# Optimization experiments

Measured on AMD Instinct MI355X. Metric: run time of the kernel, lower is better.

The kernel has to match this reference:

```python
import jax, jax.numpy as jnp
import numpy as np

B, C, H, W = 4, 256, 64, 64
C8 = C // 8


def _xavier(key, shape):
    fan_in, fan_out = shape[1], shape[0]
    limit = float(np.sqrt(6.0 / (fan_in + fan_out)))
    return jax.random.uniform(key, shape, jnp.float32, -limit, limit)


def setup_inputs() -> dict:
    key = jax.random.key(0)
    ks = jax.random.split(key, 10)
    inp = {
        "x": jax.random.normal(ks[0], (B, C, H, W), jnp.float32),
        "y": jax.random.normal(ks[1], (B, C, H, W), jnp.float32),
        "Wfx": _xavier(ks[2], (C8, C)), "bfx": jnp.zeros((C8,), jnp.float32),
        "Wgx": _xavier(ks[3], (C8, C)), "bgx": jnp.zeros((C8,), jnp.float32),
        "Whx": _xavier(ks[4], (C, C)),  "bhx": jnp.zeros((C,), jnp.float32),
        "Wfy": _xavier(ks[5], (C8, C)), "bfy": jnp.zeros((C8,), jnp.float32),
        "Wgy": _xavier(ks[6], (C8, C)), "bgy": jnp.zeros((C8,), jnp.float32),
        "Why": _xavier(ks[7], (C, C)),  "bhy": jnp.zeros((C,), jnp.float32),
        # torch init is gamma=0 which zeroes the attention branch; use a random
        # scalar so the reference exercises the full computation.
        "gamma": jax.random.normal(ks[8], (1,), jnp.float32),
    }
    return inp


def _conv1x1(x, Wt, b):
    # 1x1 conv == per-pixel linear over channels; output flattened to [B, O, N]
    b_, c, h, w = x.shape
    out = jnp.einsum('oc,bchw->bohw', Wt, x) + b[None, :, None, None]
    return out.reshape(b_, -1, h * w)


def reference(x, y, Wfx, bfx, Wgx, bgx, Whx, bhx, Wfy, bfy, Wgy, bgy, Why, bhy, gamma):
    b, c, h, w = x.shape
    fx = _conv1x1(x, Wfx, bfx)  # [B, C8, N]
    gx = _conv1x1(x, Wgx, bgx)
    hx = _conv1x1(x, Whx, bhx)  # [B, C, N]
    fy = _conv1x1(y, Wfy, bfy)
    gy = _conv1x1(y, Wgy, bgy)
    hy = _conv1x1(y, Why, bhy)

    # attention_x = softmax(f_y^T @ g_x) over last dim; [B, N, N]
    att_x = jax.nn.softmax(jnp.einsum('bcn,bcm->bnm', fy, gx), axis=-1)
    att_y = jax.nn.softmax(jnp.einsum('bcn,bcm->bnm', fx, gy), axis=-1)

    sa_x = jnp.einsum('bcn,bnm->bcm', hx, att_x).reshape(b, c, h, w)
    sa_y = jnp.einsum('bcn,bnm->bcm', hy, att_y).reshape(b, c, h, w)

    out_x = gamma[0] * sa_x + x
    out_y = gamma[0] * sa_y + y
    return (out_x, out_y)
```

## Files before the change

kernel.cpp:

```cpp
#include <hip/hip_runtime.h>

#define BB 4
#define CC 256
#define NN 4096

typedef _Float16 half_t;
typedef __attribute__((ext_vector_type(8))) _Float16 half8;
typedef __attribute__((ext_vector_type(4))) _Float16 half4;
typedef __attribute__((ext_vector_type(4))) float floatx4;
typedef __attribute__((ext_vector_type(16))) float floatx16;

__global__ __launch_bounds__(256)
void cvt_w_kernel(const float* __restrict__ Wfx, const float* __restrict__ Wgx,
                  const float* __restrict__ Whx, const float* __restrict__ Wfy,
                  const float* __restrict__ Wgy, const float* __restrict__ Why,
                  half_t* __restrict__ oWfx, half_t* __restrict__ oWgx,
                  half_t* __restrict__ oWhx, half_t* __restrict__ oWfy,
                  half_t* __restrict__ oWgy, half_t* __restrict__ oWhy)
{
    const float* src; half_t* dst; int n;
    switch (blockIdx.y) {
        case 0: src = Wfx; dst = oWfx; n = 32 * CC; break;
        case 1: src = Wgx; dst = oWgx; n = 32 * CC; break;
        case 2: src = Whx; dst = oWhx; n = CC * CC; break;
        case 3: src = Wfy; dst = oWfy; n = 32 * CC; break;
        case 4: src = Wgy; dst = oWgy; n = 32 * CC; break;
        default: src = Why; dst = oWhy; n = CC * CC; break;
    }
    int idx = (blockIdx.x * 256 + threadIdx.x) * 4;
    if (idx >= n) return;
    float4 v = *(const float4*)&src[idx];
    half4 h; h[0] = (half_t)v.x; h[1] = (half_t)v.y; h[2] = (half_t)v.z; h[3] = (half_t)v.w;
    *(half4*)&dst[idx] = h;
}

__global__ __launch_bounds__(256)
void transpose_cvt_kernel(const float* __restrict__ x, const float* __restrict__ y,
                          half_t* __restrict__ xTx, half_t* __restrict__ xTy)
{
    const int n0 = blockIdx.x * 64;
    const int c0 = blockIdx.y * 64;
    const int b  = blockIdx.z & 3;
    const int sel = blockIdx.z >> 2;
    const float* in = sel ? y : x;
    half_t* outT = sel ? xTy : xTx;
    const int t  = threadIdx.x;
    const int ch = t & 7, nl = t >> 3;
    const float* inb = in + (size_t)b * CC * NN;
    half_t* outb = outT + (size_t)b * NN * CC;

    #pragma unroll
    for (int p = 0; p < 2; ++p) {
        int n = n0 + nl + 32 * p;
        half8 hv;
        #pragma unroll
        for (int j = 0; j < 8; ++j)
            hv[j] = (half_t)inb[(size_t)(c0 + 8 * ch + j) * NN + n];
        *(half8*)&outb[(size_t)n * CC + c0 + 8 * ch] = hv;
    }
}

__global__ __launch_bounds__(256)
void proj_fg_kernel(const half_t* __restrict__ xTx, const half_t* __restrict__ xTy,
                    const half_t* __restrict__ Wfx, const half_t* __restrict__ Wgx,
                    const half_t* __restrict__ Wfy, const half_t* __restrict__ Wgy,
                    const float* __restrict__ bfx, const float* __restrict__ bgx,
                    const float* __restrict__ bfy, const float* __restrict__ bgy,
                    half_t* __restrict__ fxT, half_t* __restrict__ gxT,
                    half_t* __restrict__ fyT, half_t* __restrict__ gyT)
{
    const int n0 = blockIdx.x * 64;
    const int b  = blockIdx.y;
    const int sel = blockIdx.z;
    const half_t* xT = sel ? xTy : xTx;
    const half_t* Wf = sel ? Wfy : Wfx;
    const half_t* Wg = sel ? Wgy : Wgx;
    const float*  bf = sel ? bfy : bfx;
    const float*  bg = sel ? bgy : bgx;
    half_t* fT = sel ? fyT : fxT;
    half_t* gT = sel ? gyT : gxT;

    const int t  = threadIdx.x;
    const int w = t >> 6, lane = t & 63, q = lane >> 4, mc = lane & 15;
    const half_t* xTb = xT + (size_t)b * NN * CC;

    floatx4 acc[4];
    #pragma unroll
    for (int i = 0; i < 4; ++i) {
        float bv = (i < 2 ? bf : bg)[(i & 1) * 16 + mc];
        acc[i] = (floatx4){bv, bv, bv, bv};
    }

    #pragma unroll
    for (int ks = 0; ks < 8; ++ks) {
        int k0 = ks * 32 + q * 8;
        half8 af = *(const half8*)&xTb[(size_t)(n0 + w * 16 + mc) * CC + k0];
        #pragma unroll
        for (int i = 0; i < 4; ++i) {
            const half_t* Ws = (i < 2) ? Wf : Wg;
            half8 bfr = *(const half8*)&Ws[(size_t)((i & 1) * 16 + mc) * CC + k0];
            acc[i] = __builtin_amdgcn_mfma_f32_16x16x32_f16(af, bfr, acc[i], 0, 0, 0);
        }
    }

    #pragma unroll
    for (int i = 0; i < 4; ++i) {
        half_t* dst = (i < 2) ? fT : gT;
        #pragma unroll
        for (int r = 0; r < 4; ++r) {
            int n = n0 + w * 16 + q * 4 + r;
            dst[((size_t)b * NN + n) * 32 + (i & 1) * 16 + mc] = (half_t)acc[i][r];
        }
    }
}

__global__ __launch_bounds__(256)
void proj_h_kernel(const half_t* __restrict__ xTx, const half_t* __restrict__ xTy,
                   const half_t* __restrict__ Whx, const half_t* __restrict__ Why,
                   const float* __restrict__ bhx, const float* __restrict__ bhy,
                   half_t* __restrict__ hx, half_t* __restrict__ hy)
{
    const int n0 = blockIdx.x * 64;
    const int o0 = blockIdx.y * 128;
    const int b  = blockIdx.z & 3;
    const int sel = blockIdx.z >> 2;
    const half_t* xT = sel ? xTy : xTx;
    const half_t* Wh = sel ? Why : Whx;
    const float*  bh = sel ? bhy : bhx;
    half_t* h = sel ? hy : hx;

    const int t  = threadIdx.x;
    const int w = t >> 6, lane = t & 63, q = lane >> 4, mc = lane & 15;
    const half_t* xTb = xT + (size_t)b * NN * CC;
    half_t* hb = h + (size_t)b * CC * NN;

    floatx4 acc[2][4];
    #pragma unroll
    for (int j = 0; j < 2; ++j) {
        floatx4 bv;
        #pragma unroll
        for (int r = 0; r < 4; ++r) bv[r] = bh[o0 + w * 32 + j * 16 + q * 4 + r];
        #pragma unroll
        for (int i = 0; i < 4; ++i) acc[j][i] = bv;
    }

    #pragma unroll
    for (int ks = 0; ks < 8; ++ks) {
        int k0 = ks * 32 + q * 8;
        half8 a0 = *(const half8*)&Wh[(size_t)(o0 + w * 32 + mc) * CC + k0];
        half8 a1 = *(const half8*)&Wh[(size_t)(o0 + w * 32 + 16 + mc) * CC + k0];
        #pragma unroll
        for (int i = 0; i < 4; ++i) {
            half8 bfr = *(const half8*)&xTb[(size_t)(n0 + i * 16 + mc) * CC + k0];
            acc[0][i] = __builtin_amdgcn_mfma_f32_16x16x32_f16(a0, bfr, acc[0][i], 0, 0, 0);
            acc[1][i] = __builtin_amdgcn_mfma_f32_16x16x32_f16(a1, bfr, acc[1][i], 0, 0, 0);
        }
    }

    #pragma unroll
    for (int j = 0; j < 2; ++j)
        #pragma unroll
        for (int i = 0; i < 4; ++i)
            #pragma unroll
            for (int r = 0; r < 4; ++r) {
                int o = o0 + w * 32 + j * 16 + q * 4 + r;
                hb[(size_t)o * NN + n0 + i * 16 + mc] = (half_t)acc[j][i][r];
            }
}

__global__ __launch_bounds__(256)
void stats_kernel(const half_t* __restrict__ fT0, const half_t* __restrict__ gT0,
                  const half_t* __restrict__ fT1, const half_t* __restrict__ gT1,
                  float* __restrict__ L0, float* __restrict__ L1)
{
    __shared__ float red_l[4][32];
    const int b  = blockIdx.y;
    const int sel = blockIdx.z;
    const half_t* fT = sel ? fT1 : fT0;
    const half_t* gT = sel ? gT1 : gT0;
    float* Lout = sel ? L1 : L0;

    const int n0 = blockIdx.x * 32;
    const int t  = threadIdx.x;
    const int w = t >> 6, lane = t & 63, q = lane >> 4, mc = lane & 15;
    const half_t* fTb = fT + (size_t)b * NN * 32;
    const half_t* gTb = gT + (size_t)b * NN * 32;

    half8 a0 = *(const half8*)&fTb[(size_t)(n0 + mc) * 32 + q * 8];
    half8 a1 = *(const half8*)&fTb[(size_t)(n0 + 16 + mc) * 32 + q * 8];

    float l0[4] = {0.f, 0.f, 0.f, 0.f}, l1[4] = {0.f, 0.f, 0.f, 0.f};
    for (int it = 0; it < NN / 64; ++it) {
        int m = (it * 4 + w) * 16 + mc;
        half8 bfr = *(const half8*)&gTb[(size_t)m * 32 + q * 8];
        floatx4 S0 = __builtin_amdgcn_mfma_f32_16x16x32_f16(a0, bfr, (floatx4){0.f,0.f,0.f,0.f}, 0, 0, 0);
        floatx4 S1 = __builtin_amdgcn_mfma_f32_16x16x32_f16(a1, bfr, (floatx4){0.f,0.f,0.f,0.f}, 0, 0, 0);
        #pragma unroll
        for (int r = 0; r < 4; ++r) { l0[r] += __expf(S0[r]); l1[r] += __expf(S1[r]); }
    }
    #pragma unroll
    for (int r = 0; r < 4; ++r) {
        #pragma unroll
        for (int off = 1; off < 16; off <<= 1) {
            l0[r] += __shfl_xor(l0[r], off);
            l1[r] += __shfl_xor(l1[r], off);
        }
    }
    if (mc == 0)
        #pragma unroll
        for (int r = 0; r < 4; ++r) {
            red_l[w][q * 4 + r]      = l0[r];
            red_l[w][16 + q * 4 + r] = l1[r];
        }
    __syncthreads();
    if (t < 32) {
        float L = red_l[0][t] + red_l[1][t] + red_l[2][t] + red_l[3][t];
        Lout[(size_t)b * NN + n0 + t] = -log2f(L);
    }
}

__global__ __launch_bounds__(512, 4)
void pv_kernel(const half_t* __restrict__ fT0, const half_t* __restrict__ gT0,
               const half_t* __restrict__ h0, const float* __restrict__ L0,
               const float* __restrict__ src0, float* __restrict__ out0,
               const half_t* __restrict__ fT1, const half_t* __restrict__ gT1,
               const half_t* __restrict__ h1, const float* __restrict__ L1,
               const float* __restrict__ src1, float* __restrict__ out1,
               const float* __restrict__ gamma)
{
    __shared__ half_t h_lds[256][72];
    __shared__ half_t PT[2][64][72];

    const int m0 = blockIdx.x * 64;
    const int b  = blockIdx.y & 3;
    const int sel = blockIdx.y >> 2;
    const half_t* fT = sel ? fT1 : fT0;
    const half_t* gT = sel ? gT1 : gT0;
    const half_t* h  = sel ? h1 : h0;
    const float*  Lg = sel ? L1 : L0;
    const float*  src = sel ? src1 : src0;
    float* out = sel ? out1 : out0;

    const int t = threadIdx.x;
    const int w = t >> 6, lane = t & 63;
    const int q = lane >> 4, mc = lane & 15;
    const int l5 = lane >> 5, l31 = lane & 31;

    const int mg  = (w >> 1) * 16;
    const int nhf = (w & 1) * 32;

    const half_t* fTb = fT + (size_t)b * NN * 32;
    const half_t* gTb = gT + (size_t)b * NN * 32;
    const half_t* hb  = h + (size_t)b * CC * NN;
    const float*  Lb  = Lg + (size_t)b * NN;

    const half8 gS = *(const half8*)&gTb[(size_t)(m0 + mg + mc) * 32 + q * 8];

    const int srow = t >> 3;
    const int sch  = t & 7;

    const half_t* hP = hb + (size_t)srow * NN + sch * 8;
    const half_t* fP = fTb + (size_t)(nhf + mc) * 32 + q * 8;
    const float*  lP = Lb + nhf + q * 4;

    floatx16 acc[2];
    #pragma unroll
    for (int bm = 0; bm < 2; ++bm)
        #pragma unroll
        for (int r = 0; r < 16; ++r) acc[bm][r] = 0.f;

    half8 hpre[4];
    half8 fu[2], ff[2];
    floatx4 lvu[2], lvf[2];

    {
        half8 f0[2]; floatx4 l0[2];
        #pragma unroll
        for (int s = 0; s < 2; ++s) {
            f0[s] = *(const half8*)&fP[(size_t)(s * 16) * 32];
            l0[s] = *(const floatx4*)&lP[s * 16];
        }
        #pragma unroll
        for (int s = 0; s < 2; ++s) {
            floatx4 S = __builtin_amdgcn_mfma_f32_16x16x32_f16(
                f0[s], gS, (floatx4){0.f, 0.f, 0.f, 0.f}, 0, 0, 0);
            half4 p;
            p[0] = (half_t)exp2f(fmaf(S[0], 1.44269504f, l0[s][0]));
            p[1] = (half_t)exp2f(fmaf(S[1], 1.44269504f, l0[s][1]));
            p[2] = (half_t)exp2f(fmaf(S[2], 1.44269504f, l0[s][2]));
            p[3] = (half_t)exp2f(fmaf(S[3], 1.44269504f, l0[s][3]));
            *(half4*)&PT[0][mg + mc][nhf + s * 16 + q * 4] = p;
        }
    }
    #pragma unroll
    for (int i = 0; i < 4; ++i)
        hpre[i] = *(const half8*)&hP[(size_t)(64 * i) * NN];
    #pragma unroll
    for (int s = 0; s < 2; ++s) {
        fu[s]  = *(const half8*)&fP[(size_t)(64 + s * 16) * 32];
        lvu[s] = *(const floatx4*)&lP[64 + s * 16];
    }

    #pragma unroll 2
    for (int T = 0; T < NN / 64; ++T) {
        const int cur = T & 1, nxt = cur ^ 1;

        __syncthreads();
        #pragma unroll
        for (int i = 0; i < 4; ++i)
            *(half8*)&h_lds[srow + 64 * i][sch * 8] = hpre[i];
        __syncthreads();

        int ntn  = (T + 1) * 64; if (ntn  >= NN) ntn  = 0;
        int ntn2 = (T + 2) * 64; if (ntn2 >= NN) ntn2 -= NN;
        #pragma unroll
        for (int i = 0; i < 4; ++i)
            hpre[i] = *(const half8*)&hP[(size_t)(64 * i) * NN + ntn];
        #pragma unroll
        for (int s = 0; s < 2; ++s) {
            ff[s]  = *(const half8*)&fP[(size_t)(ntn2 + s * 16) * 32];
            lvf[s] = *(const floatx4*)&lP[ntn2 + s * 16];
        }

        #pragma unroll
        for (int s = 0; s < 2; ++s) {
            floatx4 S = __builtin_amdgcn_mfma_f32_16x16x32_f16(
                fu[s], gS, (floatx4){0.f, 0.f, 0.f, 0.f}, 0, 0, 0);
            half4 p;
            p[0] = (half_t)exp2f(fmaf(S[0], 1.44269504f, lvu[s][0]));
            p[1] = (half_t)exp2f(fmaf(S[1], 1.44269504f, lvu[s][1]));
            p[2] = (half_t)exp2f(fmaf(S[2], 1.44269504f, lvu[s][2]));
            p[3] = (half_t)exp2f(fmaf(S[3], 1.44269504f, lvu[s][3]));
            *(half4*)&PT[nxt][mg + mc][nhf + s * 16 + q * 4] = p;
        }

        __builtin_amdgcn_s_setprio(1);
        #pragma unroll
        for (int ch = 0; ch < 4; ++ch) {
            half8 Ah = *(const half8*)&h_lds[w * 32 + l31][ch * 16 + l5 * 8];
            half8 B0 = *(const half8*)&PT[cur][l31][ch * 16 + l5 * 8];
            half8 B1 = *(const half8*)&PT[cur][32 + l31][ch * 16 + l5 * 8];
            acc[0] = __builtin_amdgcn_mfma_f32_32x32x16_f16(Ah, B0, acc[0], 0, 0, 0);
            acc[1] = __builtin_amdgcn_mfma_f32_32x32x16_f16(Ah, B1, acc[1], 0, 0, 0);
        }
        __builtin_amdgcn_s_setprio(0);

        #pragma unroll
        for (int s = 0; s < 2; ++s) { fu[s] = ff[s]; lvu[s] = lvf[s]; }
    }

    const float gm = gamma[0];
    const float* srcb = src + (size_t)b * CC * NN;
    float* outb = out + (size_t)b * CC * NN;
    #pragma unroll
    for (int bm = 0; bm < 2; ++bm) {
        const int m = m0 + bm * 32 + l31;
        #pragma unroll
        for (int r = 0; r < 16; ++r) {
            int c = w * 32 + (r & 3) + 8 * (r >> 2) + 4 * l5;
            size_t idx = (size_t)c * NN + m;
            outb[idx] = fmaf(gm, acc[bm][r], srcb[idx]);
        }
    }
}

extern "C" void kernel_launch(void* const* d_in, const int* in_sizes, int n_in,
                              void* d_out, int out_size, void* d_ws, size_t ws_size,
                              hipStream_t stream)
{
    const float* x   = (const float*)d_in[0];
    const float* y   = (const float*)d_in[1];
    const float* Wfx = (const float*)d_in[2];
    const float* bfx = (const float*)d_in[3];
    const float* Wgx = (const float*)d_in[4];
    const float* bgx = (const float*)d_in[5];
    const float* Whx = (const float*)d_in[6];
    const float* bhx = (const float*)d_in[7];
    const float* Wfy = (const float*)d_in[8];
    const float* bfy = (const float*)d_in[9];
    const float* Wgy = (const float*)d_in[10];
    const float* bgy = (const float*)d_in[11];
    const float* Why = (const float*)d_in[12];
    const float* bhy = (const float*)d_in[13];
    const float* gam = (const float*)d_in[14];

    const size_t SZ_XT = (size_t)BB * NN * CC;
    const size_t SZ_FG = (size_t)BB * NN * 32;
    half_t* xTx   = (half_t*)d_ws;
    half_t* xTy   = xTx + SZ_XT;
    half_t* hx    = xTy + SZ_XT;
    half_t* hy    = hx + SZ_XT;
    half_t* fxT   = hy + SZ_XT;
    half_t* gxT   = fxT + SZ_FG;
    half_t* fyT   = gxT + SZ_FG;
    half_t* gyT   = fyT + SZ_FG;
    half_t* Wfx_h = gyT + SZ_FG;
    half_t* Wgx_h = Wfx_h + 32 * CC;
    half_t* Wfy_h = Wgx_h + 32 * CC;
    half_t* Wgy_h = Wfy_h + 32 * CC;
    half_t* Whx_h = Wgy_h + 32 * CC;
    half_t* Why_h = Whx_h + CC * CC;
    float*  Lx    = (float*)(Why_h + CC * CC);
    float*  Ly    = Lx + (size_t)BB * NN;

    float* outx = (float*)d_out;
    float* outy = outx + (size_t)BB * CC * NN;

    cvt_w_kernel<<<dim3(64, 6), 256, 0, stream>>>(Wfx, Wgx, Whx, Wfy, Wgy, Why,
                                                  Wfx_h, Wgx_h, Whx_h, Wfy_h, Wgy_h, Why_h);

    transpose_cvt_kernel<<<dim3(64, 4, 8), 256, 0, stream>>>(x, y, xTx, xTy);

    proj_fg_kernel<<<dim3(64, 4, 2), 256, 0, stream>>>(
        xTx, xTy, Wfx_h, Wgx_h, Wfy_h, Wgy_h, bfx, bgx, bfy, bgy, fxT, gxT, fyT, gyT);

    proj_h_kernel<<<dim3(64, 2, 8), 256, 0, stream>>>(
        xTx, xTy, Whx_h, Why_h, bhx, bhy, hx, hy);

    stats_kernel<<<dim3(128, 4, 2), 256, 0, stream>>>(fyT, gxT, fxT, gyT, Lx, Ly);

    pv_kernel<<<dim3(64, 8), 512, 0, stream>>>(
        fyT, gxT, hx, Lx, x, outx,
        fxT, gyT, hy, Ly, y, outy, gam);
}
```

Baseline: 282.9 us.

## Fuse transpose-convert and f/g/h projections into one LDS-staged prep kernel

Result: faster. 253.4 us (-10.4%).

```diff
diff --git a/kernel.cpp b/kernel.cpp
--- a/kernel.cpp
+++ b/kernel.cpp
@@ -34,138 +34,119 @@
     *(half4*)&dst[idx] = h;
 }
 
-__global__ __launch_bounds__(256)
-void transpose_cvt_kernel(const float* __restrict__ x, const float* __restrict__ y,
-                          half_t* __restrict__ xTx, half_t* __restrict__ xTy)
+__global__ __launch_bounds__(512, 4)
+void prep_kernel(const float* __restrict__ x, const float* __restrict__ y,
+                 const half_t* __restrict__ Wfx, const half_t* __restrict__ Wgx,
+                 const half_t* __restrict__ Whx, const half_t* __restrict__ Wfy,
+                 const half_t* __restrict__ Wgy, const half_t* __restrict__ Why,
+                 const float* __restrict__ bfx, const float* __restrict__ bgx,
+                 const float* __restrict__ bhx, const float* __restrict__ bfy,
+                 const float* __restrict__ bgy, const float* __restrict__ bhy,
+                 half_t* __restrict__ fxT, half_t* __restrict__ gxT,
+                 half_t* __restrict__ hx,
+                 half_t* __restrict__ fyT, half_t* __restrict__ gyT,
+                 half_t* __restrict__ hy)
 {
-    const int n0 = blockIdx.x * 64;
-    const int c0 = blockIdx.y * 64;
-    const int b  = blockIdx.z & 3;
-    const int sel = blockIdx.z >> 2;
-    const float* in = sel ? y : x;
-    half_t* outT = sel ? xTy : xTx;
-    const int t  = threadIdx.x;
-    const int ch = t & 7, nl = t >> 3;
-    const float* inb = in + (size_t)b * CC * NN;
-    half_t* outb = outT + (size_t)b * NN * CC;
-
-    #pragma unroll
-    for (int p = 0; p < 2; ++p) {
-        int n = n0 + nl + 32 * p;
-        half8 hv;
-        #pragma unroll
-        for (int j = 0; j < 8; ++j)
-            hv[j] = (half_t)inb[(size_t)(c0 + 8 * ch + j) * NN + n];
-        *(half8*)&outb[(size_t)n * CC + c0 + 8 * ch] = hv;
-    }
-}
-
-__global__ __launch_bounds__(256)
-void proj_fg_kernel(const half_t* __restrict__ xTx, const half_t* __restrict__ xTy,
-                    const half_t* __restrict__ Wfx, const half_t* __restrict__ Wgx,
-                    const half_t* __restrict__ Wfy, const half_t* __restrict__ Wgy,
-                    const float* __restrict__ bfx, const float* __restrict__ bgx,
-                    const float* __restrict__ bfy, const float* __restrict__ bgy,
-                    half_t* __restrict__ fxT, half_t* __restrict__ gxT,
-                    half_t* __restrict__ fyT, half_t* __restrict__ gyT)
-{
+    __shared__ half_t xT[64][266];
+
     const int n0 = blockIdx.x * 64;
     const int b  = blockIdx.y;
     const int sel = blockIdx.z;
-    const half_t* xT = sel ? xTy : xTx;
+    const float* in = sel ? y : x;
     const half_t* Wf = sel ? Wfy : Wfx;
     const half_t* Wg = sel ? Wgy : Wgx;
+    const half_t* Wh = sel ? Why : Whx;
     const float*  bf = sel ? bfy : bfx;
     const float*  bg = sel ? bgy : bgx;
+    const float*  bh = sel ? bhy : bhx;
     half_t* fT = sel ? fyT : fxT;
     half_t* gT = sel ? gyT : gxT;
-
-    const int t  = threadIdx.x;
-    const int w = t >> 6, lane = t & 63, q = lane >> 4, mc = lane & 15;
-    const half_t* xTb = xT + (size_t)b * NN * CC;
-
-    floatx4 acc[4];
-    #pragma unroll
-    for (int i = 0; i < 4; ++i) {
-        float bv = (i < 2 ? bf : bg)[(i & 1) * 16 + mc];
-        acc[i] = (floatx4){bv, bv, bv, bv};
-    }
-
-    #pragma unroll
-    for (int ks = 0; ks < 8; ++ks) {
-        int k0 = ks * 32 + q * 8;
-        half8 af = *(const half8*)&xTb[(size_t)(n0 + w * 16 + mc) * CC + k0];
-        #pragma unroll
-        for (int i = 0; i < 4; ++i) {
-            const half_t* Ws = (i < 2) ? Wf : Wg;
-            half8 bfr = *(const half8*)&Ws[(size_t)((i & 1) * 16 + mc) * CC + k0];
-            acc[i] = __builtin_amdgcn_mfma_f32_16x16x32_f16(af, bfr, acc[i], 0, 0, 0);
-        }
-    }
-
-    #pragma unroll
-    for (int i = 0; i < 4; ++i) {
-        half_t* dst = (i < 2) ? fT : gT;
-        #pragma unroll
-        for (int r = 0; r < 4; ++r) {
-            int n = n0 + w * 16 + q * 4 + r;
-            dst[((size_t)b * NN + n) * 32 + (i & 1) * 16 + mc] = (half_t)acc[i][r];
-        }
-    }
-}
-
-__global__ __launch_bounds__(256)
-void proj_h_kernel(const half_t* __restrict__ xTx, const half_t* __restrict__ xTy,
-                   const half_t* __restrict__ Whx, const half_t* __restrict__ Why,
-                   const float* __restrict__ bhx, const float* __restrict__ bhy,
-                   half_t* __restrict__ hx, half_t* __restrict__ hy)
-{
-    const int n0 = blockIdx.x * 64;
-    const int o0 = blockIdx.y * 128;
-    const int b  = blockIdx.z & 3;
-    const int sel = blockIdx.z >> 2;
-    const half_t* xT = sel ? xTy : xTx;
-    const half_t* Wh = sel ? Why : Whx;
-    const float*  bh = sel ? bhy : bhx;
-    half_t* h = sel ? hy : hx;
-
-    const int t  = threadIdx.x;
-    const int w = t >> 6, lane = t & 63, q = lane >> 4, mc = lane & 15;
-    const half_t* xTb = xT + (size_t)b * NN * CC;
-    half_t* hb = h + (size_t)b * CC * NN;
-
-    floatx4 acc[2][4];
-    #pragma unroll
-    for (int j = 0; j < 2; ++j) {
-        floatx4 bv;
-        #pragma unroll
-        for (int r = 0; r < 4; ++r) bv[r] = bh[o0 + w * 32 + j * 16 + q * 4 + r];
-        #pragma unroll
-        for (int i = 0; i < 4; ++i) acc[j][i] = bv;
-    }
-
-    #pragma unroll
-    for (int ks = 0; ks < 8; ++ks) {
-        int k0 = ks * 32 + q * 8;
-        half8 a0 = *(const half8*)&Wh[(size_t)(o0 + w * 32 + mc) * CC + k0];
-        half8 a1 = *(const half8*)&Wh[(size_t)(o0 + w * 32 + 16 + mc) * CC + k0];
-        #pragma unroll
-        for (int i = 0; i < 4; ++i) {
-            half8 bfr = *(const half8*)&xTb[(size_t)(n0 + i * 16 + mc) * CC + k0];
-            acc[0][i] = __builtin_amdgcn_mfma_f32_16x16x32_f16(a0, bfr, acc[0][i], 0, 0, 0);
-            acc[1][i] = __builtin_amdgcn_mfma_f32_16x16x32_f16(a1, bfr, acc[1][i], 0, 0, 0);
-        }
-    }
-
-    #pragma unroll
-    for (int j = 0; j < 2; ++j)
-        #pragma unroll
-        for (int i = 0; i < 4; ++i)
+    half_t* h  = sel ? hy : hx;
+
+    const int t = threadIdx.x;
+    const int w = t >> 6, lane = t & 63;
+    const int q = lane >> 4, mc = lane & 15;
+
+    {
+        const int n4 = t & 15;
+        const int cb = t >> 4;
+        const float* inb = in + (size_t)b * CC * NN + n0 + n4 * 4;
+        #pragma unroll
+        for (int j = 0; j < 8; ++j) {
+            const int c = cb + 32 * j;
+            float4 v = *(const float4*)&inb[(size_t)c * NN];
+            xT[n4 * 4 + 0][c] = (half_t)v.x;
+            xT[n4 * 4 + 1][c] = (half_t)v.y;
+            xT[n4 * 4 + 2][c] = (half_t)v.z;
+            xT[n4 * 4 + 3][c] = (half_t)v.w;
+        }
+    }
+    __syncthreads();
+
+    {
+        const int of  = w >> 1;
+        const int col = (of & 1) * 16 + mc;
+        const half_t* Ws = (of < 2) ? Wf : Wg;
+        const float*  bs = (of < 2) ? bf : bg;
+        half_t* dst = (of < 2) ? fT : gT;
+        const float bv = bs[col];
+        floatx4 accf[2] = {{bv, bv, bv, bv}, {bv, bv, bv, bv}};
+
+        #pragma unroll
+        for (int ks = 0; ks < 8; ++ks) {
+            int k0 = ks * 32 + q * 8;
+            half8 bfr = *(const half8*)&Ws[(size_t)col * CC + k0];
+            #pragma unroll
+            for (int e = 0; e < 2; ++e) {
+                half8 af = *(const half8*)&xT[(w & 1) * 32 + e * 16 + mc][k0];
+                accf[e] = __builtin_amdgcn_mfma_f32_16x16x32_f16(af, bfr, accf[e], 0, 0, 0);
+            }
+        }
+        #pragma unroll
+        for (int e = 0; e < 2; ++e)
             #pragma unroll
             for (int r = 0; r < 4; ++r) {
-                int o = o0 + w * 32 + j * 16 + q * 4 + r;
-                hb[(size_t)o * NN + n0 + i * 16 + mc] = (half_t)acc[j][i][r];
+                int n = n0 + (w & 1) * 32 + e * 16 + q * 4 + r;
+                dst[((size_t)b * NN + n) * 32 + col] = (half_t)accf[e][r];
             }
+    }
+
+    {
+        const int o0 = w * 32;
+        floatx4 acch[2][4];
+        #pragma unroll
+        for (int j = 0; j < 2; ++j) {
+            floatx4 bv;
+            #pragma unroll
+            for (int r = 0; r < 4; ++r) bv[r] = bh[o0 + j * 16 + q * 4 + r];
+            #pragma unroll
+            for (int i = 0; i < 4; ++i) acch[j][i] = bv;
+        }
+
+        #pragma unroll
+        for (int ks = 0; ks < 8; ++ks) {
+            int k0 = ks * 32 + q * 8;
+            half8 a0 = *(const half8*)&Wh[(size_t)(o0 + mc) * CC + k0];
+            half8 a1 = *(const half8*)&Wh[(size_t)(o0 + 16 + mc) * CC + k0];
+            #pragma unroll
+            for (int i = 0; i < 4; ++i) {
+                half8 bfr = *(const half8*)&xT[i * 16 + mc][k0];
+                acch[0][i] = __builtin_amdgcn_mfma_f32_16x16x32_f16(a0, bfr, acch[0][i], 0, 0, 0);
+                acch[1][i] = __builtin_amdgcn_mfma_f32_16x16x32_f16(a1, bfr, acch[1][i], 0, 0, 0);
+            }
+        }
+
+        half_t* hb = h + (size_t)b * CC * NN;
+        #pragma unroll
+        for (int j = 0; j < 2; ++j)
+            #pragma unroll
+            for (int i = 0; i < 4; ++i)
+                #pragma unroll
+                for (int r = 0; r < 4; ++r) {
+                    int o = o0 + j * 16 + q * 4 + r;
+                    hb[(size_t)o * NN + n0 + i * 16 + mc] = (half_t)acch[j][i][r];
+                }
+    }
 }
 
 __global__ __launch_bounds__(256)
@@ -409,13 +390,10 @@
     cvt_w_kernel<<<dim3(64, 6), 256, 0, stream>>>(Wfx, Wgx, Whx, Wfy, Wgy, Why,
                                                   Wfx_h, Wgx_h, Whx_h, Wfy_h, Wgy_h, Why_h);
 
-    transpose_cvt_kernel<<<dim3(64, 4, 8), 256, 0, stream>>>(x, y, xTx, xTy);
-
-    proj_fg_kernel<<<dim3(64, 4, 2), 256, 0, stream>>>(
-        xTx, xTy, Wfx_h, Wgx_h, Wfy_h, Wgy_h, bfx, bgx, bfy, bgy, fxT, gxT, fyT, gyT);
-
-    proj_h_kernel<<<dim3(64, 2, 8), 256, 0, stream>>>(
-        xTx, xTy, Whx_h, Why_h, bhx, bhy, hx, hy);
+    prep_kernel<<<dim3(64, 4, 2), 512, 0, stream>>>(
+        x, y, Wfx_h, Wgx_h, Whx_h, Wfy_h, Wgy_h, Why_h,
+        bfx, bgx, bhx, bfy, bgy, bhy,
+        fxT, gxT, hx, fyT, gyT, hy);
 
     stats_kernel<<<dim3(128, 4, 2), 256, 0, stream>>>(fyT, gxT, fxT, gyT, Lx, Ly);
 
```
